# Kernel optimization log

Measured on AMD Instinct MI355X. Metric: run time of the kernel, lower is better.

The kernel has to match this reference:

```python
import jax, jax.numpy as jnp
import numpy as np

# MACE-style symmetric contraction (single scalar output irrep, correlation nu=3)
B, C, I, E = 2048, 128, 16, 10          # nodes, channels, irrep feature dim (0e+1o+2e+3o), n species
K3, K2, K1 = 11, 4, 1                   # num CG paths at correlation 3, 2, 1


def setup_inputs() -> dict:
    key = jax.random.key(0)
    ks = jax.random.split(key, 8)
    x = jax.random.normal(ks[0], (B, C, I), jnp.float32)
    y = jax.random.normal(ks[1], (B, E), jnp.float32)  # argmax'd -> species index (stand-in for one-hot)
    # U tensors: generalized Clebsch-Gordan bases (constant buffers in MACE); random stand-ins with correct shapes
    U3 = jax.random.normal(ks[2], (I, I, I, K3), jnp.float32) * 0.1
    U2 = jax.random.normal(ks[3], (I, I, K2), jnp.float32) * 0.1
    U1 = jax.random.normal(ks[4], (I, K1), jnp.float32) * 0.1
    # per-species learned weights [E, K, C]
    W3 = jax.random.normal(ks[5], (E, K3, C), jnp.float32) / np.sqrt(K3)
    W2 = jax.random.normal(ks[6], (E, K2, C), jnp.float32) / np.sqrt(K2)
    W1 = jax.random.normal(ks[7], (E, K1, C), jnp.float32) / np.sqrt(K1)
    return dict(x=x, y=y, U3=U3, U2=U2, U1=U1, W3=W3, W2=W2, W1=W1)


def reference(x, y, U3, U2, U1, W3, W2, W1):
    # wrapper: species index from (one-hot-like) y
    idx = jnp.argmax(y, axis=-1)                       # [B] int
    w3, w2, w1 = W3[idx], W2[idx], W1[idx]             # gather per-node weights: [B,K,C]

    # main term (correlation 3): out[b,c,p,q] = sum_{i,k} U3[p,q,i,k] * w3[b,k,c] * x[b,c,i]
    # (MACE equation '...ik,ekc,bci,be->bc...' with one-hot replaced by gather)
    z = jnp.einsum('bkc,bci->bcik', w3, x)             # [B,C,I,K3] outer product, no contraction
    out = jnp.einsum('pqik,bcik->bcpq', U3, z)         # GEMM: (B*C) x (I*K3) x (I*I)

    # correlation 2: weighting '...k,ekc,be->bc...' then contract 'bc...i,bci->bc...'
    c2 = jnp.einsum('pik,bkc->bcpi', U2, w2) + out     # [B,C,I,I]
    out = jnp.einsum('bcpi,bci->bcp', c2, x)           # [B,C,I]

    # correlation 1
    c1 = jnp.einsum('ik,bkc->bci', U1, w1) + out       # [B,C,I]
    out = jnp.einsum('bci,bci->bc', c1, x)             # [B,C]  (already squeezed, matches .squeeze())
    return out
```

## Files before the change

kernel.cpp:

```cpp
#include <hip/hip_runtime.h>
#include <hip/hip_bf16.h>
#include <utility>

typedef __fp16 h2    __attribute__((ext_vector_type(2)));
typedef __fp16 v8h   __attribute__((ext_vector_type(8)));
typedef _Float16 v8f16 __attribute__((ext_vector_type(8)));
typedef float  v4f   __attribute__((ext_vector_type(4)));
typedef float  v16f  __attribute__((ext_vector_type(16)));

#define NT 5
#define KTSTRIDE (NT * 64 * 8)
#define NCHUNK (12 * NT * 64)

__device__ __forceinline__ short h16(float f) {
    return __builtin_bit_cast(short, (_Float16)f);
}

__device__ __forceinline__ void gload16(const short* g, short* l) {
    __builtin_amdgcn_global_load_lds(
        (const __attribute__((address_space(1))) unsigned int*)g,
        (__attribute__((address_space(3))) unsigned int*)l, 16, 0, 0);
}

__device__ __forceinline__ v8h pack4(h2 a, h2 b, h2 c, h2 d) {
    union { int4 i; v8h h; } u;
    u.i = make_int4(__builtin_bit_cast(int, a), __builtin_bit_cast(int, b),
                    __builtin_bit_cast(int, c), __builtin_bit_cast(int, d));
    return u.h;
}

__device__ __forceinline__ v16f mfma_f16(v8h a, v8h b, v16f c) {
    return __builtin_amdgcn_mfma_f32_32x32x16_f16(
        __builtin_bit_cast(v8f16, a), __builtin_bit_cast(v8f16, b), c, 0, 0, 0);
}

constexpr int pof(int n) {
    int p = 0, b = 0;
    while (b + (16 - p) <= n) { b += 16 - p; ++p; }
    return p;
}
constexpr int qof(int n) {
    int p = 0, b = 0;
    while (b + (16 - p) <= n) { b += 16 - p; ++p; }
    return p + (n - b);
}

template<int I>
__device__ __forceinline__ float xi(v4f f0, v4f f1, v4f f2, v4f f3) {
    if constexpr (I < 4)       return f0[I];
    else if constexpr (I < 8)  return f1[I - 4];
    else if constexpr (I < 12) return f2[I - 8];
    else                       return f3[I - 12];
}

template<int N>
__device__ __forceinline__ float gg(v4f f0, v4f f1, v4f f2, v4f f3) {
    if constexpr (N >= 136) return 0.f;
    else return xi<pof(N)>(f0, f1, f2, f3) * xi<qof(N)>(f0, f1, f2, f3);
}

template<int NTI, int... RG>
__device__ __forceinline__ float epi_impl(const v16f& a, v4f f0, v4f f1, v4f f2, v4f f3,
                                          int h, std::integer_sequence<int, RG...>) {
    float s = 0.f;
    ((s = fmaf(a[RG],
               h ? gg<NTI * 32 + (RG & 3) + 8 * (RG >> 2) + 4>(f0, f1, f2, f3)
                 : gg<NTI * 32 + (RG & 3) + 8 * (RG >> 2)>(f0, f1, f2, f3),
               s)), ...);
    return s;
}
template<int NTI>
__device__ __forceinline__ float epi(const v16f& a, v4f f0, v4f f1, v4f f2, v4f f3, int h) {
    return epi_impl<NTI>(a, f0, f1, f2, f3, h, std::make_integer_sequence<int, 16>{});
}

__global__ void symcon_prep(const float* __restrict__ U3, const float* __restrict__ U2,
                            short* __restrict__ Bg)
{
    const int g = blockIdx.x * 256 + threadIdx.x;
    if (g >= 160 * 16) return;
    const int n = g >> 4;
    const int i = g & 15;
    const int nt = n >> 5, lb = n & 31;
    const int lane = lb | ((i >> 3) << 5), j = i & 7;
    short* dst = Bg + (nt * 64 + lane) * 8 + j;
    if (n < 136) {
        int p = 0, base = 0;
        while (base + (16 - p) <= n) { base += 16 - p; ++p; }
        const int q = p + (n - base);
        const float* up = U3 + ((p * 16 + q) * 16 + i) * 11;
        const float* uq = U3 + ((q * 16 + p) * 16 + i) * 11;
        #pragma unroll
        for (int k3 = 0; k3 < 11; ++k3)
            dst[k3 * KTSTRIDE] = h16(up[k3] + (p != q ? uq[k3] : 0.f));
        if (i == 0) {
            short* d0 = Bg + 11 * KTSTRIDE + (nt * 64 + lb) * 8;
            #pragma unroll
            for (int jj = 0; jj < 4; ++jj)
                d0[jj] = h16(U2[(p * 16 + q) * 4 + jj] + (p != q ? U2[(q * 16 + p) * 4 + jj] : 0.f));
            #pragma unroll
            for (int jj = 4; jj < 8; ++jj) d0[jj] = 0;
            short* d1 = Bg + 11 * KTSTRIDE + (nt * 64 + lb + 32) * 8;
            #pragma unroll
            for (int jj = 0; jj < 8; ++jj) d1[jj] = 0;
        }
    } else {
        #pragma unroll
        for (int k3 = 0; k3 < 11; ++k3) dst[k3 * KTSTRIDE] = 0;
        if (i == 0) {
            short* d0 = Bg + 11 * KTSTRIDE + (nt * 64 + lb) * 8;
            short* d1 = Bg + 11 * KTSTRIDE + (nt * 64 + lb + 32) * 8;
            #pragma unroll
            for (int jj = 0; jj < 8; ++jj) { d0[jj] = 0; d1[jj] = 0; }
        }
    }
}

__global__ __launch_bounds__(512, 4)
void symcon_main(const float* __restrict__ x, const float* __restrict__ y,
                 const float* __restrict__ U1, const float* __restrict__ W3,
                 const float* __restrict__ W2, const float* __restrict__ W1,
                 const short* __restrict__ Bg, float* __restrict__ out)
{
    __shared__ __align__(16) short Ul[NCHUNK * 8];

    const int tid  = threadIdx.x;
    const int lane = tid & 63;
    const int wid  = tid >> 6;
    const int node = blockIdx.x * 2 + (wid >> 2);
    const int wr   = wid & 3;
    const int col  = lane & 31;
    const int h    = lane >> 5;
    const int m    = wr * 32 + col;

    #pragma unroll
    for (int jj = 0; jj < 7; ++jj) {
        const int c = ((jj * 8 + wid) << 6) + lane;
        gload16(Bg + c * 8, &Ul[c * 8]);
    }
    if (wid < 4) {
        const int c = ((56 + wid) << 6) + lane;
        gload16(Bg + c * 8, &Ul[c * 8]);
    }

    const float* xp = x + ((size_t)node * 128 + m) * 16;
    const v4f f0 = *reinterpret_cast<const v4f*>(xp);
    const v4f f1 = *reinterpret_cast<const v4f*>(xp + 4);
    const v4f f2 = *reinterpret_cast<const v4f*>(xp + 8);
    const v4f f3 = *reinterpret_cast<const v4f*>(xp + 12);

    int e = 0;
    {
        const float* yr = y + node * 10;
        float best = yr[0];
        #pragma unroll
        for (int s2 = 1; s2 < 10; ++s2) { const float v = yr[s2]; if (v > best) { best = v; e = s2; } }
    }

    float u1dot;
    {
        const v4f u0 = *reinterpret_cast<const v4f*>(U1);
        const v4f u1 = *reinterpret_cast<const v4f*>(U1 + 4);
        const v4f u2 = *reinterpret_cast<const v4f*>(U1 + 8);
        const v4f u3 = *reinterpret_cast<const v4f*>(U1 + 12);
        const v4f d  = f0 * u0 + f1 * u1 + f2 * u2 + f3 * u3;
        u1dot = d[0] + d[1] + d[2] + d[3];
    }

    float w3r[11], w2r[4];
    #pragma unroll
    for (int k = 0; k < 11; ++k) w3r[k] = W3[(e * 11 + k) * 128 + m];
    #pragma unroll
    for (int k = 0; k < 4; ++k)  w2r[k] = W2[(e * 4 + k) * 128 + m];
    const float w1v = W1[e * 128 + m];

    const v4f lo = h ? f2 : f0;
    const v4f hi = h ? f3 : f1;
    const h2 xh0 = h2{(__fp16)lo[0], (__fp16)lo[1]};
    const h2 xh1 = h2{(__fp16)lo[2], (__fp16)lo[3]};
    const h2 xh2 = h2{(__fp16)hi[0], (__fp16)hi[1]};
    const h2 xh3 = h2{(__fp16)hi[2], (__fp16)hi[3]};

    __syncthreads();

    v16f a0 = {}, a1 = {}, a2 = {}, a3 = {}, a4 = {};

    const short* Up = Ul + lane * 8;
    #pragma unroll
    for (int kt = 0; kt < 12; ++kt) {
        const v8h u0 = *reinterpret_cast<const v8h*>(Up + (kt * NT + 0) * 512);
        const v8h u1 = *reinterpret_cast<const v8h*>(Up + (kt * NT + 1) * 512);
        const v8h u2 = *reinterpret_cast<const v8h*>(Up + (kt * NT + 2) * 512);
        const v8h u3 = *reinterpret_cast<const v8h*>(Up + (kt * NT + 3) * 512);
        const v8h u4 = *reinterpret_cast<const v8h*>(Up + (kt * NT + 4) * 512);
        v8h b;
        if (kt < 11) {
            const __fp16 w = (__fp16)w3r[kt];
            const h2 wh = h2{w, w};
            b = pack4(xh0 * wh, xh1 * wh, xh2 * wh, xh3 * wh);
        } else {
            const h2 z = {};
            const h2 p0 = h ? z : h2{(__fp16)w2r[0], (__fp16)w2r[1]};
            const h2 p1 = h ? z : h2{(__fp16)w2r[2], (__fp16)w2r[3]};
            b = pack4(p0, p1, z, z);
        }
        a0 = mfma_f16(u0, b, a0);
        a1 = mfma_f16(u1, b, a1);
        a2 = mfma_f16(u2, b, a2);
        a3 = mfma_f16(u3, b, a3);
        a4 = mfma_f16(u4, b, a4);
    }

    float s = epi<0>(a0, f0, f1, f2, f3, h)
            + epi<1>(a1, f0, f1, f2, f3, h)
            + epi<2>(a2, f0, f1, f2, f3, h)
            + epi<3>(a3, f0, f1, f2, f3, h)
            + epi<4>(a4, f0, f1, f2, f3, h);

    s += __shfl_xor(s, 32);

    if (h == 0)
        out[(size_t)node * 128 + m] = s + w1v * u1dot;
}

extern "C" void kernel_launch(void* const* d_in, const int* in_sizes, int n_in,
                              void* d_out, int out_size, void* d_ws, size_t ws_size,
                              hipStream_t stream) {
    const float* x  = (const float*)d_in[0];
    const float* y  = (const float*)d_in[1];
    const float* U3 = (const float*)d_in[2];
    const float* U2 = (const float*)d_in[3];
    const float* U1 = (const float*)d_in[4];
    const float* W3 = (const float*)d_in[5];
    const float* W2 = (const float*)d_in[6];
    const float* W1 = (const float*)d_in[7];
    short* Bg = (short*)d_ws;

    symcon_prep<<<10, 256, 0, stream>>>(U3, U2, Bg);
    symcon_main<<<1024, 512, 0, stream>>>(x, y, U1, W3, W2, W1, Bg, (float*)d_out);
}
```

Before: 26.97 us.

## Process two 32-channel tiles per wave to reuse LDS U fragments

Each wave now handles 64 channels (two MFMA B operands) instead of 32, so every U fragment read from LDS feeds two MFMAs. Blocks shrink to 256 threads with the same two nodes per block, halving the waves per block and the LDS reads per MFMA. The cost is double the accumulator registers (10 v16f) and lower occupancy, and the epilogue reloads x from global memory instead of keeping it in registers.

Result: slower. 28.47 us (+5.5%).

```diff
diff --git a/kernel.cpp b/kernel.cpp
--- a/kernel.cpp
+++ b/kernel.cpp
@@ -116,7 +116,7 @@
     }
 }
 
-__global__ __launch_bounds__(512, 4)
+__global__ __launch_bounds__(256, 2)
 void symcon_main(const float* __restrict__ x, const float* __restrict__ y,
                  const float* __restrict__ U1, const float* __restrict__ W3,
                  const float* __restrict__ W2, const float* __restrict__ W1,
@@ -127,27 +127,18 @@
     const int tid  = threadIdx.x;
     const int lane = tid & 63;
     const int wid  = tid >> 6;
-    const int node = blockIdx.x * 2 + (wid >> 2);
-    const int wr   = wid & 3;
+    const int node = blockIdx.x * 2 + (wid >> 1);
+    const int chp  = wid & 1;
     const int col  = lane & 31;
     const int h    = lane >> 5;
-    const int m    = wr * 32 + col;
-
-    #pragma unroll
-    for (int jj = 0; jj < 7; ++jj) {
-        const int c = ((jj * 8 + wid) << 6) + lane;
+    const int m0   = chp * 64 + col;
+    const int m1   = m0 + 32;
+
+    #pragma unroll
+    for (int jj = 0; jj < 15; ++jj) {
+        const int c = jj * 256 + tid;
         gload16(Bg + c * 8, &Ul[c * 8]);
     }
-    if (wid < 4) {
-        const int c = ((56 + wid) << 6) + lane;
-        gload16(Bg + c * 8, &Ul[c * 8]);
-    }
-
-    const float* xp = x + ((size_t)node * 128 + m) * 16;
-    const v4f f0 = *reinterpret_cast<const v4f*>(xp);
-    const v4f f1 = *reinterpret_cast<const v4f*>(xp + 4);
-    const v4f f2 = *reinterpret_cast<const v4f*>(xp + 8);
-    const v4f f3 = *reinterpret_cast<const v4f*>(xp + 12);
 
     int e = 0;
     {
@@ -157,70 +148,108 @@
         for (int s2 = 1; s2 < 10; ++s2) { const float v = yr[s2]; if (v > best) { best = v; e = s2; } }
     }
 
-    float u1dot;
-    {
-        const v4f u0 = *reinterpret_cast<const v4f*>(U1);
-        const v4f u1 = *reinterpret_cast<const v4f*>(U1 + 4);
-        const v4f u2 = *reinterpret_cast<const v4f*>(U1 + 8);
-        const v4f u3 = *reinterpret_cast<const v4f*>(U1 + 12);
-        const v4f d  = f0 * u0 + f1 * u1 + f2 * u2 + f3 * u3;
-        u1dot = d[0] + d[1] + d[2] + d[3];
-    }
-
-    float w3r[11], w2r[4];
-    #pragma unroll
-    for (int k = 0; k < 11; ++k) w3r[k] = W3[(e * 11 + k) * 128 + m];
-    #pragma unroll
-    for (int k = 0; k < 4; ++k)  w2r[k] = W2[(e * 4 + k) * 128 + m];
-    const float w1v = W1[e * 128 + m];
-
-    const v4f lo = h ? f2 : f0;
-    const v4f hi = h ? f3 : f1;
-    const h2 xh0 = h2{(__fp16)lo[0], (__fp16)lo[1]};
-    const h2 xh1 = h2{(__fp16)lo[2], (__fp16)lo[3]};
-    const h2 xh2 = h2{(__fp16)hi[0], (__fp16)hi[1]};
-    const h2 xh3 = h2{(__fp16)hi[2], (__fp16)hi[3]};
+    h2 xh0[4], xh1[4];
+    {
+        const float* xb = x + ((size_t)node * 128) * 16;
+        const v4f lo0 = *reinterpret_cast<const v4f*>(xb + m0 * 16 + h * 8);
+        const v4f hi0 = *reinterpret_cast<const v4f*>(xb + m0 * 16 + h * 8 + 4);
+        const v4f lo1 = *reinterpret_cast<const v4f*>(xb + m1 * 16 + h * 8);
+        const v4f hi1 = *reinterpret_cast<const v4f*>(xb + m1 * 16 + h * 8 + 4);
+        xh0[0] = h2{(__fp16)lo0[0], (__fp16)lo0[1]};
+        xh0[1] = h2{(__fp16)lo0[2], (__fp16)lo0[3]};
+        xh0[2] = h2{(__fp16)hi0[0], (__fp16)hi0[1]};
+        xh0[3] = h2{(__fp16)hi0[2], (__fp16)hi0[3]};
+        xh1[0] = h2{(__fp16)lo1[0], (__fp16)lo1[1]};
+        xh1[1] = h2{(__fp16)lo1[2], (__fp16)lo1[3]};
+        xh1[2] = h2{(__fp16)hi1[0], (__fp16)hi1[1]};
+        xh1[3] = h2{(__fp16)hi1[2], (__fp16)hi1[3]};
+    }
+
+    float w3a[11], w3b[11], w2a[4], w2b[4];
+    #pragma unroll
+    for (int k = 0; k < 11; ++k) {
+        w3a[k] = W3[(e * 11 + k) * 128 + m0];
+        w3b[k] = W3[(e * 11 + k) * 128 + m1];
+    }
+    #pragma unroll
+    for (int k = 0; k < 4; ++k) {
+        w2a[k] = W2[(e * 4 + k) * 128 + m0];
+        w2b[k] = W2[(e * 4 + k) * 128 + m1];
+    }
 
     __syncthreads();
 
-    v16f a0 = {}, a1 = {}, a2 = {}, a3 = {}, a4 = {};
+    v16f aA[NT] = {}, aB[NT] = {};
 
     const short* Up = Ul + lane * 8;
     #pragma unroll
     for (int kt = 0; kt < 12; ++kt) {
-        const v8h u0 = *reinterpret_cast<const v8h*>(Up + (kt * NT + 0) * 512);
-        const v8h u1 = *reinterpret_cast<const v8h*>(Up + (kt * NT + 1) * 512);
-        const v8h u2 = *reinterpret_cast<const v8h*>(Up + (kt * NT + 2) * 512);
-        const v8h u3 = *reinterpret_cast<const v8h*>(Up + (kt * NT + 3) * 512);
-        const v8h u4 = *reinterpret_cast<const v8h*>(Up + (kt * NT + 4) * 512);
-        v8h b;
+        v8h u[NT];
+        #pragma unroll
+        for (int t = 0; t < NT; ++t)
+            u[t] = *reinterpret_cast<const v8h*>(Up + (kt * NT + t) * 512);
+        v8h b0, b1;
         if (kt < 11) {
-            const __fp16 w = (__fp16)w3r[kt];
-            const h2 wh = h2{w, w};
-            b = pack4(xh0 * wh, xh1 * wh, xh2 * wh, xh3 * wh);
+            const __fp16 wa = (__fp16)w3a[kt];
+            const __fp16 wb = (__fp16)w3b[kt];
+            const h2 wha = h2{wa, wa};
+            const h2 whb = h2{wb, wb};
+            b0 = pack4(xh0[0] * wha, xh0[1] * wha, xh0[2] * wha, xh0[3] * wha);
+            b1 = pack4(xh1[0] * whb, xh1[1] * whb, xh1[2] * whb, xh1[3] * whb);
         } else {
             const h2 z = {};
-            const h2 p0 = h ? z : h2{(__fp16)w2r[0], (__fp16)w2r[1]};
-            const h2 p1 = h ? z : h2{(__fp16)w2r[2], (__fp16)w2r[3]};
-            b = pack4(p0, p1, z, z);
-        }
-        a0 = mfma_f16(u0, b, a0);
-        a1 = mfma_f16(u1, b, a1);
-        a2 = mfma_f16(u2, b, a2);
-        a3 = mfma_f16(u3, b, a3);
-        a4 = mfma_f16(u4, b, a4);
-    }
-
-    float s = epi<0>(a0, f0, f1, f2, f3, h)
-            + epi<1>(a1, f0, f1, f2, f3, h)
-            + epi<2>(a2, f0, f1, f2, f3, h)
-            + epi<3>(a3, f0, f1, f2, f3, h)
-            + epi<4>(a4, f0, f1, f2, f3, h);
-
-    s += __shfl_xor(s, 32);
-
-    if (h == 0)
-        out[(size_t)node * 128 + m] = s + w1v * u1dot;
+            const h2 p00 = h ? z : h2{(__fp16)w2a[0], (__fp16)w2a[1]};
+            const h2 p01 = h ? z : h2{(__fp16)w2a[2], (__fp16)w2a[3]};
+            const h2 p10 = h ? z : h2{(__fp16)w2b[0], (__fp16)w2b[1]};
+            const h2 p11 = h ? z : h2{(__fp16)w2b[2], (__fp16)w2b[3]};
+            b0 = pack4(p00, p01, z, z);
+            b1 = pack4(p10, p11, z, z);
+        }
+        #pragma unroll
+        for (int t = 0; t < NT; ++t) {
+            aA[t] = mfma_f16(u[t], b0, aA[t]);
+            aB[t] = mfma_f16(u[t], b1, aB[t]);
+        }
+    }
+
+    const v4f u1q0 = *reinterpret_cast<const v4f*>(U1);
+    const v4f u1q1 = *reinterpret_cast<const v4f*>(U1 + 4);
+    const v4f u1q2 = *reinterpret_cast<const v4f*>(U1 + 8);
+    const v4f u1q3 = *reinterpret_cast<const v4f*>(U1 + 12);
+
+    float s0, s1, lin0, lin1;
+    {
+        const float* xp = x + ((size_t)node * 128 + m0) * 16;
+        const v4f f0 = *reinterpret_cast<const v4f*>(xp);
+        const v4f f1 = *reinterpret_cast<const v4f*>(xp + 4);
+        const v4f f2 = *reinterpret_cast<const v4f*>(xp + 8);
+        const v4f f3 = *reinterpret_cast<const v4f*>(xp + 12);
+        s0 = epi<0>(aA[0], f0, f1, f2, f3, h) + epi<1>(aA[1], f0, f1, f2, f3, h)
+           + epi<2>(aA[2], f0, f1, f2, f3, h) + epi<3>(aA[3], f0, f1, f2, f3, h)
+           + epi<4>(aA[4], f0, f1, f2, f3, h);
+        const v4f d = f0 * u1q0 + f1 * u1q1 + f2 * u1q2 + f3 * u1q3;
+        lin0 = (d[0] + d[1] + d[2] + d[3]) * W1[e * 128 + m0];
+    }
+    {
+        const float* xp = x + ((size_t)node * 128 + m1) * 16;
+        const v4f f0 = *reinterpret_cast<const v4f*>(xp);
+        const v4f f1 = *reinterpret_cast<const v4f*>(xp + 4);
+        const v4f f2 = *reinterpret_cast<const v4f*>(xp + 8);
+        const v4f f3 = *reinterpret_cast<const v4f*>(xp + 12);
+        s1 = epi<0>(aB[0], f0, f1, f2, f3, h) + epi<1>(aB[1], f0, f1, f2, f3, h)
+           + epi<2>(aB[2], f0, f1, f2, f3, h) + epi<3>(aB[3], f0, f1, f2, f3, h)
+           + epi<4>(aB[4], f0, f1, f2, f3, h);
+        const v4f d = f0 * u1q0 + f1 * u1q1 + f2 * u1q2 + f3 * u1q3;
+        lin1 = (d[0] + d[1] + d[2] + d[3]) * W1[e * 128 + m1];
+    }
+
+    s0 += __shfl_xor(s0, 32);
+    s1 += __shfl_xor(s1, 32);
+
+    if (h == 0) {
+        out[(size_t)node * 128 + m0] = s0 + lin0;
+        out[(size_t)node * 128 + m1] = s1 + lin1;
+    }
 }
 
 extern "C" void kernel_launch(void* const* d_in, const int* in_sizes, int n_in,
@@ -237,5 +266,5 @@
     short* Bg = (short*)d_ws;
 
     symcon_prep<<<10, 256, 0, stream>>>(U3, U2, Bg);
-    symcon_main<<<1024, 512, 0, stream>>>(x, y, U1, W3, W2, W1, Bg, (float*)d_out);
-}
+    symcon_main<<<1024, 256, 0, stream>>>(x, y, U1, W3, W2, W1, Bg, (float*)d_out);
+}
```

## Process two node pairs per block, move argmax to prep, split epilogue by half

Applied to the files above, without the earlier changes.

Each block now handles four nodes in two sequential passes and loads the shared U basis into LDS only once, halving the grid and the per-node LDS staging cost. The species argmax is moved into the prep kernel and written to workspace. The epilogue uses compile-time branches on the lane half with packed two-wide float math. s_setprio is raised around the MFMA group. Risks include lower parallelism with only 512 blocks, extra serial latency inside each block, and extra registers.

Result: slower. 28.86 us (+7.0%).

```diff
diff --git a/kernel.cpp b/kernel.cpp
--- a/kernel.cpp
+++ b/kernel.cpp
@@ -5,6 +5,7 @@
 typedef __fp16 h2    __attribute__((ext_vector_type(2)));
 typedef __fp16 v8h   __attribute__((ext_vector_type(8)));
 typedef _Float16 v8f16 __attribute__((ext_vector_type(8)));
+typedef float  v2f   __attribute__((ext_vector_type(2)));
 typedef float  v4f   __attribute__((ext_vector_type(4)));
 typedef float  v16f  __attribute__((ext_vector_type(16)));
 
@@ -53,71 +54,88 @@
     else                       return f3[I - 12];
 }
 
-template<int N>
-__device__ __forceinline__ float gg(v4f f0, v4f f1, v4f f2, v4f f3) {
-    if constexpr (N >= 136) return 0.f;
-    else return xi<pof(N)>(f0, f1, f2, f3) * xi<qof(N)>(f0, f1, f2, f3);
-}
-
-template<int NTI, int... RG>
-__device__ __forceinline__ float epi_impl(const v16f& a, v4f f0, v4f f1, v4f f2, v4f f3,
-                                          int h, std::integer_sequence<int, RG...>) {
-    float s = 0.f;
-    ((s = fmaf(a[RG],
-               h ? gg<NTI * 32 + (RG & 3) + 8 * (RG >> 2) + 4>(f0, f1, f2, f3)
-                 : gg<NTI * 32 + (RG & 3) + 8 * (RG >> 2)>(f0, f1, f2, f3),
-               s)), ...);
-    return s;
-}
-template<int NTI>
-__device__ __forceinline__ float epi(const v16f& a, v4f f0, v4f f1, v4f f2, v4f f3, int h) {
-    return epi_impl<NTI>(a, f0, f1, f2, f3, h, std::make_integer_sequence<int, 16>{});
+template<int NTI, int H, int R2>
+__device__ __forceinline__ void pair2(v2f& s2, const v16f& a,
+                                      v4f f0, v4f f1, v4f f2, v4f f3) {
+    constexpr int rgp = 2 * R2;
+    constexpr int N0 = NTI * 32 + (rgp & 3) + 8 * (rgp >> 2) + 4 * H;
+    if constexpr (N0 < 136) {
+        v2f xp2, xq2, a2;
+        xp2[0] = xi<pof(N0)>(f0, f1, f2, f3);
+        xq2[0] = xi<qof(N0)>(f0, f1, f2, f3);
+        if constexpr (N0 + 1 < 136) {
+            xp2[1] = xi<pof(N0 + 1)>(f0, f1, f2, f3);
+            xq2[1] = xi<qof(N0 + 1)>(f0, f1, f2, f3);
+        } else { xp2[1] = 0.f; xq2[1] = 0.f; }
+        a2[0] = a[rgp]; a2[1] = a[rgp + 1];
+        s2 += a2 * (xp2 * xq2);
+    }
+}
+
+template<int NTI, int H, int... R2>
+__device__ __forceinline__ void epi2_impl(v2f& s2, const v16f& a, v4f f0, v4f f1,
+                                          v4f f2, v4f f3,
+                                          std::integer_sequence<int, R2...>) {
+    ((pair2<NTI, H, R2>(s2, a, f0, f1, f2, f3)), ...);
+}
+template<int NTI, int H>
+__device__ __forceinline__ void epi2(v2f& s2, const v16f& a, v4f f0, v4f f1,
+                                     v4f f2, v4f f3) {
+    epi2_impl<NTI, H>(s2, a, f0, f1, f2, f3, std::make_integer_sequence<int, 8>{});
 }
 
 __global__ void symcon_prep(const float* __restrict__ U3, const float* __restrict__ U2,
-                            short* __restrict__ Bg)
+                            const float* __restrict__ y, short* __restrict__ Bg)
 {
     const int g = blockIdx.x * 256 + threadIdx.x;
-    if (g >= 160 * 16) return;
-    const int n = g >> 4;
-    const int i = g & 15;
-    const int nt = n >> 5, lb = n & 31;
-    const int lane = lb | ((i >> 3) << 5), j = i & 7;
-    short* dst = Bg + (nt * 64 + lane) * 8 + j;
-    if (n < 136) {
-        int p = 0, base = 0;
-        while (base + (16 - p) <= n) { base += 16 - p; ++p; }
-        const int q = p + (n - base);
-        const float* up = U3 + ((p * 16 + q) * 16 + i) * 11;
-        const float* uq = U3 + ((q * 16 + p) * 16 + i) * 11;
-        #pragma unroll
-        for (int k3 = 0; k3 < 11; ++k3)
-            dst[k3 * KTSTRIDE] = h16(up[k3] + (p != q ? uq[k3] : 0.f));
-        if (i == 0) {
-            short* d0 = Bg + 11 * KTSTRIDE + (nt * 64 + lb) * 8;
+    if (g < 2560) {
+        const int n = g >> 4;
+        const int i = g & 15;
+        const int nt = n >> 5, lb = n & 31;
+        const int lane = lb | ((i >> 3) << 5), j = i & 7;
+        short* dst = Bg + (nt * 64 + lane) * 8 + j;
+        if (n < 136) {
+            int p = 0, base = 0;
+            while (base + (16 - p) <= n) { base += 16 - p; ++p; }
+            const int q = p + (n - base);
+            const float* up = U3 + ((p * 16 + q) * 16 + i) * 11;
+            const float* uq = U3 + ((q * 16 + p) * 16 + i) * 11;
             #pragma unroll
-            for (int jj = 0; jj < 4; ++jj)
-                d0[jj] = h16(U2[(p * 16 + q) * 4 + jj] + (p != q ? U2[(q * 16 + p) * 4 + jj] : 0.f));
+            for (int k3 = 0; k3 < 11; ++k3)
+                dst[k3 * KTSTRIDE] = h16(up[k3] + (p != q ? uq[k3] : 0.f));
+            if (i == 0) {
+                short* d0 = Bg + 11 * KTSTRIDE + (nt * 64 + lb) * 8;
+                #pragma unroll
+                for (int jj = 0; jj < 4; ++jj)
+                    d0[jj] = h16(U2[(p * 16 + q) * 4 + jj] + (p != q ? U2[(q * 16 + p) * 4 + jj] : 0.f));
+                #pragma unroll
+                for (int jj = 4; jj < 8; ++jj) d0[jj] = 0;
+                short* d1 = Bg + 11 * KTSTRIDE + (nt * 64 + lb + 32) * 8;
+                #pragma unroll
+                for (int jj = 0; jj < 8; ++jj) d1[jj] = 0;
+            }
+        } else {
             #pragma unroll
-            for (int jj = 4; jj < 8; ++jj) d0[jj] = 0;
-            short* d1 = Bg + 11 * KTSTRIDE + (nt * 64 + lb + 32) * 8;
-            #pragma unroll
-            for (int jj = 0; jj < 8; ++jj) d1[jj] = 0;
-        }
-    } else {
-        #pragma unroll
-        for (int k3 = 0; k3 < 11; ++k3) dst[k3 * KTSTRIDE] = 0;
-        if (i == 0) {
-            short* d0 = Bg + 11 * KTSTRIDE + (nt * 64 + lb) * 8;
-            short* d1 = Bg + 11 * KTSTRIDE + (nt * 64 + lb + 32) * 8;
-            #pragma unroll
-            for (int jj = 0; jj < 8; ++jj) { d0[jj] = 0; d1[jj] = 0; }
-        }
+            for (int k3 = 0; k3 < 11; ++k3) dst[k3 * KTSTRIDE] = 0;
+            if (i == 0) {
+                short* d0 = Bg + 11 * KTSTRIDE + (nt * 64 + lb) * 8;
+                short* d1 = Bg + 11 * KTSTRIDE + (nt * 64 + lb + 32) * 8;
+                #pragma unroll
+                for (int jj = 0; jj < 8; ++jj) { d0[jj] = 0; d1[jj] = 0; }
+            }
+        }
+    } else if (g < 2560 + 2048) {
+        const int node = g - 2560;
+        const float* yr = y + node * 10;
+        int e = 0; float best = yr[0];
+        #pragma unroll
+        for (int s2 = 1; s2 < 10; ++s2) { const float v = yr[s2]; if (v > best) { best = v; e = s2; } }
+        ((int*)(Bg + 12 * KTSTRIDE))[node] = e;
     }
 }
 
 __global__ __launch_bounds__(512, 4)
-void symcon_main(const float* __restrict__ x, const float* __restrict__ y,
+void symcon_main(const float* __restrict__ x,
                  const float* __restrict__ U1, const float* __restrict__ W3,
                  const float* __restrict__ W2, const float* __restrict__ W1,
                  const short* __restrict__ Bg, float* __restrict__ out)
@@ -127,11 +145,11 @@
     const int tid  = threadIdx.x;
     const int lane = tid & 63;
     const int wid  = tid >> 6;
-    const int node = blockIdx.x * 2 + (wid >> 2);
-    const int wr   = wid & 3;
     const int col  = lane & 31;
     const int h    = lane >> 5;
+    const int wr   = wid & 3;
     const int m    = wr * 32 + col;
+    const int* eA  = (const int*)(Bg + 12 * KTSTRIDE);
 
     #pragma unroll
     for (int jj = 0; jj < 7; ++jj) {
@@ -143,84 +161,98 @@
         gload16(Bg + c * 8, &Ul[c * 8]);
     }
 
-    const float* xp = x + ((size_t)node * 128 + m) * 16;
-    const v4f f0 = *reinterpret_cast<const v4f*>(xp);
-    const v4f f1 = *reinterpret_cast<const v4f*>(xp + 4);
-    const v4f f2 = *reinterpret_cast<const v4f*>(xp + 8);
-    const v4f f3 = *reinterpret_cast<const v4f*>(xp + 12);
-
-    int e = 0;
-    {
-        const float* yr = y + node * 10;
-        float best = yr[0];
-        #pragma unroll
-        for (int s2 = 1; s2 < 10; ++s2) { const float v = yr[s2]; if (v > best) { best = v; e = s2; } }
-    }
-
-    float u1dot;
-    {
-        const v4f u0 = *reinterpret_cast<const v4f*>(U1);
-        const v4f u1 = *reinterpret_cast<const v4f*>(U1 + 4);
-        const v4f u2 = *reinterpret_cast<const v4f*>(U1 + 8);
-        const v4f u3 = *reinterpret_cast<const v4f*>(U1 + 12);
-        const v4f d  = f0 * u0 + f1 * u1 + f2 * u2 + f3 * u3;
-        u1dot = d[0] + d[1] + d[2] + d[3];
-    }
-
-    float w3r[11], w2r[4];
+    __syncthreads();
+
+    const short* Up = Ul + lane * 8;
+
     #pragma unroll
-    for (int k = 0; k < 11; ++k) w3r[k] = W3[(e * 11 + k) * 128 + m];
-    #pragma unroll
-    for (int k = 0; k < 4; ++k)  w2r[k] = W2[(e * 4 + k) * 128 + m];
-    const float w1v = W1[e * 128 + m];
-
-    const v4f lo = h ? f2 : f0;
-    const v4f hi = h ? f3 : f1;
-    const h2 xh0 = h2{(__fp16)lo[0], (__fp16)lo[1]};
-    const h2 xh1 = h2{(__fp16)lo[2], (__fp16)lo[3]};
-    const h2 xh2 = h2{(__fp16)hi[0], (__fp16)hi[1]};
-    const h2 xh3 = h2{(__fp16)hi[2], (__fp16)hi[3]};
-
-    __syncthreads();
-
-    v16f a0 = {}, a1 = {}, a2 = {}, a3 = {}, a4 = {};
-
-    const short* Up = Ul + lane * 8;
-    #pragma unroll
-    for (int kt = 0; kt < 12; ++kt) {
-        const v8h u0 = *reinterpret_cast<const v8h*>(Up + (kt * NT + 0) * 512);
-        const v8h u1 = *reinterpret_cast<const v8h*>(Up + (kt * NT + 1) * 512);
-        const v8h u2 = *reinterpret_cast<const v8h*>(Up + (kt * NT + 2) * 512);
-        const v8h u3 = *reinterpret_cast<const v8h*>(Up + (kt * NT + 3) * 512);
-        const v8h u4 = *reinterpret_cast<const v8h*>(Up + (kt * NT + 4) * 512);
-        v8h b;
-        if (kt < 11) {
-            const __fp16 w = (__fp16)w3r[kt];
-            const h2 wh = h2{w, w};
-            b = pack4(xh0 * wh, xh1 * wh, xh2 * wh, xh3 * wh);
+    for (int j = 0; j < 2; ++j) {
+        const int node = (blockIdx.x * 2 + j) * 2 + (wid >> 2);
+        const int e    = eA[node];
+
+        const float* xp = x + ((size_t)node * 128 + m) * 16;
+        h2 xh[4];
+        {
+            const v4f lo = *reinterpret_cast<const v4f*>(xp + h * 8);
+            const v4f hi = *reinterpret_cast<const v4f*>(xp + h * 8 + 4);
+            xh[0] = h2{(__fp16)lo[0], (__fp16)lo[1]};
+            xh[1] = h2{(__fp16)lo[2], (__fp16)lo[3]};
+            xh[2] = h2{(__fp16)hi[0], (__fp16)hi[1]};
+            xh[3] = h2{(__fp16)hi[2], (__fp16)hi[3]};
+        }
+
+        float w3r[11], w2r[4];
+        #pragma unroll
+        for (int k = 0; k < 11; ++k) w3r[k] = W3[(e * 11 + k) * 128 + m];
+        #pragma unroll
+        for (int k = 0; k < 4; ++k)  w2r[k] = W2[(e * 4 + k) * 128 + m];
+        const float w1v = W1[e * 128 + m];
+
+        v16f a0 = {}, a1 = {}, a2 = {}, a3 = {}, a4 = {};
+
+        #pragma unroll
+        for (int kt = 0; kt < 12; ++kt) {
+            const v8h u0 = *reinterpret_cast<const v8h*>(Up + (kt * NT + 0) * 512);
+            const v8h u1 = *reinterpret_cast<const v8h*>(Up + (kt * NT + 1) * 512);
+            const v8h u2 = *reinterpret_cast<const v8h*>(Up + (kt * NT + 2) * 512);
+            const v8h u3 = *reinterpret_cast<const v8h*>(Up + (kt * NT + 3) * 512);
+            const v8h u4 = *reinterpret_cast<const v8h*>(Up + (kt * NT + 4) * 512);
+            v8h b;
+            if (kt < 11) {
+                const __fp16 w = (__fp16)w3r[kt];
+                const h2 wh = h2{w, w};
+                b = pack4(xh[0] * wh, xh[1] * wh, xh[2] * wh, xh[3] * wh);
+            } else {
+                const h2 z = {};
+                const h2 p0 = h ? z : h2{(__fp16)w2r[0], (__fp16)w2r[1]};
+                const h2 p1 = h ? z : h2{(__fp16)w2r[2], (__fp16)w2r[3]};
+                b = pack4(p0, p1, z, z);
+            }
+            __builtin_amdgcn_s_setprio(1);
+            a0 = mfma_f16(u0, b, a0);
+            a1 = mfma_f16(u1, b, a1);
+            a2 = mfma_f16(u2, b, a2);
+            a3 = mfma_f16(u3, b, a3);
+            a4 = mfma_f16(u4, b, a4);
+            __builtin_amdgcn_s_setprio(0);
+        }
+
+        const v4f f0 = *reinterpret_cast<const v4f*>(xp);
+        const v4f f1 = *reinterpret_cast<const v4f*>(xp + 4);
+        const v4f f2 = *reinterpret_cast<const v4f*>(xp + 8);
+        const v4f f3 = *reinterpret_cast<const v4f*>(xp + 12);
+
+        v2f s2 = {0.f, 0.f};
+        if (h == 0) {
+            epi2<0, 0>(s2, a0, f0, f1, f2, f3);
+            epi2<1, 0>(s2, a1, f0, f1, f2, f3);
+            epi2<2, 0>(s2, a2, f0, f1, f2, f3);
+            epi2<3, 0>(s2, a3, f0, f1, f2, f3);
+            epi2<4, 0>(s2, a4, f0, f1, f2, f3);
         } else {
-            const h2 z = {};
-            const h2 p0 = h ? z : h2{(__fp16)w2r[0], (__fp16)w2r[1]};
-            const h2 p1 = h ? z : h2{(__fp16)w2r[2], (__fp16)w2r[3]};
-            b = pack4(p0, p1, z, z);
-        }
-        a0 = mfma_f16(u0, b, a0);
-        a1 = mfma_f16(u1, b, a1);
-        a2 = mfma_f16(u2, b, a2);
-        a3 = mfma_f16(u3, b, a3);
-        a4 = mfma_f16(u4, b, a4);
-    }
-
-    float s = epi<0>(a0, f0, f1, f2, f3, h)
-            + epi<1>(a1, f0, f1, f2, f3, h)
-            + epi<2>(a2, f0, f1, f2, f3, h)
-            + epi<3>(a3, f0, f1, f2, f3, h)
-            + epi<4>(a4, f0, f1, f2, f3, h);
-
-    s += __shfl_xor(s, 32);
-
-    if (h == 0)
-        out[(size_t)node * 128 + m] = s + w1v * u1dot;
+            epi2<0, 1>(s2, a0, f0, f1, f2, f3);
+            epi2<1, 1>(s2, a1, f0, f1, f2, f3);
+            epi2<2, 1>(s2, a2, f0, f1, f2, f3);
+            epi2<3, 1>(s2, a3, f0, f1, f2, f3);
+            epi2<4, 1>(s2, a4, f0, f1, f2, f3);
+        }
+        float s = s2[0] + s2[1];
+
+        float u1dot;
+        {
+            const v4f u0q = *reinterpret_cast<const v4f*>(U1);
+            const v4f u1q = *reinterpret_cast<const v4f*>(U1 + 4);
+            const v4f u2q = *reinterpret_cast<const v4f*>(U1 + 8);
+            const v4f u3q = *reinterpret_cast<const v4f*>(U1 + 12);
+            const v4f d = f0 * u0q + f1 * u1q + f2 * u2q + f3 * u3q;
+            u1dot = d[0] + d[1] + d[2] + d[3];
+        }
+
+        s += __shfl_xor(s, 32);
+
+        if (h == 0)
+            out[(size_t)node * 128 + m] = s + w1v * u1dot;
+    }
 }
 
 extern "C" void kernel_launch(void* const* d_in, const int* in_sizes, int n_in,
@@ -236,6 +268,6 @@
     const float* W1 = (const float*)d_in[7];
     short* Bg = (short*)d_ws;
 
-    symcon_prep<<<10, 256, 0, stream>>>(U3, U2, Bg);
-    symcon_main<<<1024, 512, 0, stream>>>(x, y, U1, W3, W2, W1, Bg, (float*)d_out);
-}
+    symcon_prep<<<18, 256, 0, stream>>>(U3, U2, y, Bg);
+    symcon_main<<<512, 512, 0, stream>>>(x, U1, W3, W2, W1, Bg, (float*)d_out);
+}
```
